# Optimization experiments

Hardware: AMD Instinct MI355X
Metric: run time of the kernel (lower is better)

Reference implementation:

```python
import jax, jax.numpy as jnp
import numpy as np
from jax import lax

# ---- config (mirrors cfg) ----
NUM_LEVELS = 4
DS = 2            # DS_FACTOR
T = 16            # TILE_SIZE
SR = 4            # SEARCH_RADIUS
PADD = 1
SW = 0.1          # SPATIAL_WEIGHT
GR = 2            # GAUSS_RADIUS
SIGMA = 1.0
SS = 2 * (SR + PADD) + 1      # 11: padded search grid
SSC = 2 * SR + 1              # 9: cropped search grid
WIN = T + 2 * (SR + PADD)     # 26: gathered window per tile

# ---- subpixel-refinement quadratic-fit filters (from __init__) ----
F_A11 = jnp.asarray(np.array([[1,-2,1],[2,-4,2],[1,-2,1]], np.float32) / 4.0)
F_A22 = jnp.asarray(np.array([[1,2,1],[-2,-4,-2],[1,2,1]], np.float32) / 4.0)
F_A12 = jnp.asarray(np.array([[1,0,-1],[0,0,0],[-1,0,1]], np.float32) / 4.0)
F_B1  = jnp.asarray(np.array([[-1,0,1],[-2,0,2],[-1,0,1]], np.float32) / 8.0)
F_B2  = jnp.asarray(np.array([[-1,-2,-1],[0,0,0],[1,2,1]], np.float32) / 8.0)
F_C   = jnp.asarray(np.array([[-1,2,-1],[2,12,2],[-1,2,-1]], np.float32) / 16.0)


def _gauss_kernel():
    ws = 2 * GR + 1
    ax = np.arange(ws, dtype=np.float32) - GR
    g = np.exp(-(ax ** 2) / (2.0 * SIGMA ** 2))
    k = np.outer(g, g)
    k = k / k.sum()
    return jnp.asarray(k, jnp.float32)


def _pyramid(x):
    """Gaussian pyramid: depthwise gaussian blur + avg-pool(ds) per level."""
    k = _gauss_kernel()[None, None]  # OIHW, C=1
    pad = (2 * GR + 1 - 1) // 2
    pyr = [x]
    for _ in range(NUM_LEVELS - 1):
        y = lax.conv_general_dilated(x, k, (1, 1), [(pad, pad), (pad, pad)],
                                     dimension_numbers=('NCHW', 'OIHW', 'NCHW'))
        n, c, h, w = y.shape
        x = y.reshape(n, c, h // DS, DS, w // DS, DS).mean(axis=(3, 5))
        pyr.append(x)
    return pyr


def _sdist_map():
    ax = (np.arange(SS, dtype=np.float32) - (SR + PADD)) / float(SS)
    return jnp.asarray(ax[:, None] ** 2 + ax[None, :] ** 2, jnp.float32)


def _step(init_offset, src, dst):
    """One pyramid-level block-matching step + subpixel refine."""
    n, nth, ntw, _ = init_offset.shape
    H, W = src.shape[2], src.shape[3]
    oy = jnp.round(init_offset[..., 0]).astype(jnp.int32)
    ox = jnp.round(init_offset[..., 1]).astype(jnp.int32)
    base_y = (jnp.arange(nth, dtype=jnp.int32) * T)[None, :, None]
    base_x = (jnp.arange(ntw, dtype=jnp.int32) * T)[None, None, :]
    y0 = base_y + oy - (SR + PADD)
    x0 = base_x + ox - (SR + PADD)
    Y = jnp.clip(y0[..., None] + jnp.arange(WIN), 0, H - 1)
    X = jnp.clip(x0[..., None] + jnp.arange(WIN), 0, W - 1)
    nidx = jnp.arange(n)[:, None, None, None, None]
    window = dst[:, 0][nidx, Y[..., :, None], X[..., None, :]]
    # source tiles [n,nth,ntw,T,T]
    src_t = src[:, 0].reshape(n, nth, T, ntw, T).transpose(0, 1, 3, 2, 4)
    # all SSxSS candidate tiles from the window (static slide indices)
    sl = jnp.arange(SS)[:, None] + jnp.arange(T)[None, :]  # [SS,T]
    cand = window[:, :, :, sl[:, None, :, None], sl[None, :, None, :]]  # [n,nth,ntw,SS,SS,T,T]
    adist = jnp.mean((cand - src_t[:, :, :, None, None]) ** 2, axis=(-2, -1))
    dist_full = adist + SW * _sdist_map()  # [n,nth,ntw,SS,SS]
    dist = dist_full[:, :, :, PADD:-PADD, PADD:-PADD].reshape(n, nth, ntw, SSC * SSC)
    min_dist = jnp.min(dist, axis=3)
    pk = jnp.argmin(dist, axis=3)
    py = pk // SSC
    px = pk % SSC
    offset = init_offset + jnp.stack([(py - SR).astype(jnp.float32),
                                      (px - SR).astype(jnp.float32)], axis=3)
    # RegionSelection: 3x3 neighborhood of dist_full around (py+PADD, px+PADD)
    ry = (py + PADD)[..., None] + jnp.arange(-1, 2)
    rx = (px + PADD)[..., None] + jnp.arange(-1, 2)
    tyi = jnp.arange(nth)[None, :, None, None, None]
    txi = jnp.arange(ntw)[None, None, :, None, None]
    yreg = dist_full[nidx, tyi, txi, ry[..., :, None], rx[..., None, :]]  # [n,nth,ntw,3,3]
    s = lambda f: jnp.sum(f * yreg, axis=(-2, -1))
    a11 = jax.nn.relu(s(F_A11))
    a22 = jax.nn.relu(s(F_A22))
    a12 = s(F_A12)
    b1 = s(F_B1)
    b2 = s(F_B2)
    det = a11 * a22 - a12 ** 2
    a12z = jnp.where(det < 0, jnp.zeros_like(a12), a12)
    mu_x = -(a22 * b1 - a12z * b2) / det
    mu_y = -(a11 * b2 - a12z * b1) / det
    mu_len = jnp.sqrt(mu_y ** 2 + mu_x ** 2)
    dx = jnp.where(mu_len < 1.0, mu_x, jnp.zeros_like(mu_x))
    dy = jnp.where(mu_len < 1.0, mu_y, jnp.zeros_like(mu_y))
    offset = offset.at[..., 0].add(dy).at[..., 1].add(dx)
    return offset, min_dist


def _inherit(prev_offset, nth, ntw, H, W):
    typ = jnp.arange(nth) // DS
    txp = jnp.arange(ntw) // DS
    off = DS * prev_offset[:, typ[:, None], txp[None, :], :]
    iy = (jnp.arange(nth, dtype=jnp.float32) * T)[None, :, None]
    ix = (jnp.arange(ntw, dtype=jnp.float32) * T)[None, None, :]
    dy = jnp.clip(off[..., 0] + iy, 0.0, float(H - T)) - iy
    dx = jnp.clip(off[..., 1] + ix, 0.0, float(W - T)) - ix
    return jnp.round(jnp.stack([dy, dx], axis=3))


def _align(src, dst):
    ps = _pyramid(src)
    pd = _pyramid(dst)
    offset = None
    min_dist = None
    for level in range(NUM_LEVELS - 1, -1, -1):
        s, d = ps[level], pd[level]
        n, _, h, w = s.shape
        nth = int(np.ceil(h / T))
        ntw = int(np.ceil(w / T))
        if level == NUM_LEVELS - 1:
            init = jnp.zeros((n, nth, ntw, 2), jnp.float32)
        else:
            init = _inherit(offset, nth, ntw, h, w)
        offset, min_dist = _step(init, s, d)
    # nearest-neighbor upsample by TILE_SIZE to per-pixel maps
    pixel_off = jnp.repeat(jnp.repeat(offset, T, axis=1), T, axis=2)   # [n,H,W,2]
    pixel_dist = jnp.repeat(jnp.repeat(min_dist, T, axis=1), T, axis=2)  # [n,H,W]
    return pixel_off, pixel_dist


def setup_inputs() -> dict:
    key = jax.random.key(0)
    k1, k2 = jax.random.split(key)
    src = jax.random.uniform(k1, (4, 1, 512, 512), jnp.float32)
    dst = jax.random.uniform(k2, (4, 1, 512, 512), jnp.float32)
    return {"src": src, "dst": dst}


def reference(src, dst):
    return _align(src, dst)
```

## Files before the change

### kernel.cpp

```cpp
#include <hip/hip_runtime.h>


#define NB 4

constexpr float H6[6] = {
    0.027244342f, 0.149345013f, 0.323410645f,
    0.323410645f, 0.149345013f, 0.027244342f
};

__global__ void __launch_bounds__(256, 2)
pyramid_kernel(const float* __restrict__ src, const float* __restrict__ dst,
               float* __restrict__ ws) {
    __shared__ float smem[14652];
    float* patch = smem;
    float* tmpH  = smem + 9900;
    float* l1    = smem;
    float* tmpB  = smem + 2256;
    float* l2    = smem + 9900;
    float* tmp3  = smem + 3384;

    float* sL1 = ws;
    float* dL1 = sL1 + 4 * 65536;
    float* sL2 = dL1 + 4 * 65536;
    float* dL2 = sL2 + 4 * 16384;
    float* sL3 = dL2 + 4 * 16384;
    float* dL3 = sL3 + 4 * 4096;

    const int bx = blockIdx.x, by = blockIdx.y, z = blockIdx.z;
    const int t = threadIdx.x;

    const float* in = (z < 4) ? (src + (size_t)z * 262144) : (dst + (size_t)(z - 4) * 262144);
    float* outL1 = ((z < 4) ? sL1 : dL1) + (size_t)(z & 3) * 65536;
    float* outL2 = ((z < 4) ? sL2 : dL2) + (size_t)(z & 3) * 16384;
    float* outL3 = ((z < 4) ? sL3 : dL3) + (size_t)(z & 3) * 4096;

    {
        const int oy = by * 64 - 14, ox = bx * 64 - 14;
        for (int idx = t; idx < 99 * 99; idx += 256) {
            int r = idx / 99, c = idx - r * 99;
            int gy = oy + r, gx = ox + c;
            float v = 0.0f;
            if (gy >= 0 && gy < 512 && gx >= 0 && gx < 512) v = in[gy * 512 + gx];
            patch[r * 100 + c] = v;
        }
    }
    __syncthreads();
    for (int idx = t; idx < 99 * 47; idx += 256) {
        int r = idx / 47, v = idx - r * 47;
        const float* p = &patch[r * 100 + 2 * v];
        float a = 0.f;
        #pragma unroll
        for (int b = 0; b < 6; ++b) a = fmaf(H6[b], p[b], a);
        tmpH[r * 48 + v] = a;
    }
    __syncthreads();
    {
        const int oy = by * 32 - 6, ox = bx * 32 - 6;
        for (int idx = t; idx < 47 * 47; idx += 256) {
            int u = idx / 47, v = idx - u * 47;
            float a = 0.f;
            int y1 = oy + u, x1 = ox + v;
            if (y1 >= 0 && y1 < 256 && x1 >= 0 && x1 < 256) {
                #pragma unroll
                for (int b = 0; b < 6; ++b) a = fmaf(H6[b], tmpH[(2 * u + b) * 48 + v], a);
            }
            l1[u * 48 + v] = a;
        }
    }
    __syncthreads();
    for (int idx = t; idx < 1024; idx += 256) {
        int u = idx >> 5, v = idx & 31;
        outL1[(by * 32 + u) * 256 + bx * 32 + v] = l1[(6 + u) * 48 + 6 + v];
    }
    for (int idx = t; idx < 47 * 21; idx += 256) {
        int r = idx / 21, v = idx - r * 21;
        const float* p = &l1[r * 48 + 2 * v];
        float a = 0.f;
        #pragma unroll
        for (int b = 0; b < 6; ++b) a = fmaf(H6[b], p[b], a);
        tmpB[r * 24 + v] = a;
    }
    __syncthreads();
    {
        const int oy = by * 16 - 2, ox = bx * 16 - 2;
        for (int idx = t; idx < 21 * 21; idx += 256) {
            int u = idx / 21, v = idx - u * 21;
            float a = 0.f;
            int y2 = oy + u, x2 = ox + v;
            if (y2 >= 0 && y2 < 128 && x2 >= 0 && x2 < 128) {
                #pragma unroll
                for (int b = 0; b < 6; ++b) a = fmaf(H6[b], tmpB[(2 * u + b) * 24 + v], a);
            }
            l2[u * 24 + v] = a;
        }
    }
    __syncthreads();
    for (int idx = t; idx < 256; idx += 256) {
        int u = idx >> 4, v = idx & 15;
        outL2[(by * 16 + u) * 128 + bx * 16 + v] = l2[(2 + u) * 24 + 2 + v];
    }
    for (int idx = t; idx < 21 * 8; idx += 256) {
        int r = idx >> 3, v = idx & 7;
        const float* p = &l2[r * 24 + 2 * v];
        float a = 0.f;
        #pragma unroll
        for (int b = 0; b < 6; ++b) a = fmaf(H6[b], p[b], a);
        tmp3[r * 8 + v] = a;
    }
    __syncthreads();
    if (t < 64) {
        int u = t >> 3, v = t & 7;
        float a = 0.f;
        #pragma unroll
        for (int b = 0; b < 6; ++b) a = fmaf(H6[b], tmp3[(2 * u + b) * 8 + v], a);
        outL3[(by * 8 + u) * 64 + bx * 8 + v] = a;
    }
}

__global__ void __launch_bounds__(256, 4)
step_chain_kernel(const float* __restrict__ src, const float* __restrict__ dst,
                  const float* __restrict__ ws, float* __restrict__ out) {
    __shared__ float winS[2][26 * 28];
    __shared__ float stS[2][256];
    __shared__ float distS[2][128];
    __shared__ float offLv[4][2];
    __shared__ float resY[2], resX[2], resD[2];

    const float* sL1 = ws;
    const float* dL1 = sL1 + 4 * 65536;
    const float* sL2 = dL1 + 4 * 65536;
    const float* dL2 = sL2 + 4 * 16384;
    const float* sL3 = dL2 + 4 * 16384;
    const float* dL3 = sL3 + 4 * 4096;

    const int gid = blockIdx.x;
    const int b   = gid >> 8;
    const int ty1 = (gid >> 4) & 15;
    const int tx1 = gid & 15;
    const int t    = threadIdx.x;
    const int slot = t >> 7;
    const int s_t  = t & 127;
    const int NPIX = NB * 512 * 512;

    float* win  = winS[slot];
    float* st   = stS[slot];
    float* dist = distS[slot];

    #pragma unroll 1
    for (int round = 0; round < 5; ++round) {
        int lvl, ty, tx; bool act, hasPar;
        const float* simg; const float* dimg; int H;
        switch (round) {
            case 0: lvl = 3; ty = ty1 >> 2; tx = tx1 >> 2; act = (slot == 0); hasPar = false; break;
            case 1: lvl = 2; ty = ty1 >> 1; tx = tx1 >> 1; act = (slot == 0); hasPar = true;  break;
            case 2: lvl = 1; ty = ty1;      tx = tx1;      act = (slot == 0); hasPar = true;  break;
            case 3: lvl = 0; ty = 2 * ty1;     tx = 2 * tx1 + slot; act = true; hasPar = true; break;
            default:lvl = 0; ty = 2 * ty1 + 1; tx = 2 * tx1 + slot; act = true; hasPar = true; break;
        }
        switch (lvl) {
            case 0: simg = src + (size_t)b * 262144; dimg = dst + (size_t)b * 262144; H = 512; break;
            case 1: simg = sL1 + (size_t)b * 65536;  dimg = dL1 + (size_t)b * 65536;  H = 256; break;
            case 2: simg = sL2 + (size_t)b * 16384;  dimg = dL2 + (size_t)b * 16384;  H = 128; break;
            default:simg = sL3 + (size_t)b * 4096;   dimg = dL3 + (size_t)b * 4096;   H = 64;  break;
        }

        float dyf = 0.f, dxf = 0.f;
        if (hasPar) {
            float poy = offLv[lvl + 1][0], pox = offLv[lvl + 1][1];
            float iy = (float)(ty * 16), ix = (float)(tx * 16);
            dyf = rintf(fminf(fmaxf(2.f * poy + iy, 0.f), (float)(H - 16)) - iy);
            dxf = rintf(fminf(fmaxf(2.f * pox + ix, 0.f), (float)(H - 16)) - ix);
        }
        const int ioy = (int)dyf, iox = (int)dxf;

        if (act) {
            const int y0 = ty * 16 + ioy - 5;
            const int x0 = tx * 16 + iox - 5;
            for (int idx = s_t; idx < 26 * 26; idx += 128) {
                int r = idx / 26, c = idx - r * 26;
                int gy = min(max(y0 + r, 0), H - 1);
                int gx = min(max(x0 + c, 0), H - 1);
                win[r * 28 + c] = dimg[gy * H + gx];
            }
            if (s_t < 64) {
                int r = s_t >> 2, q = s_t & 3;
                const float4* srow = (const float4*)(simg + (size_t)(ty * 16 + r) * H + tx * 16);
                ((float4*)&st[r * 16])[q] = srow[q];
            }
        }
        __syncthreads();

        if (act) {
            const int dy = s_t >> 3;
            const int dyc = min(dy, 10);
            float acc[11];
            #pragma unroll
            for (int q = 0; q < 11; ++q) acc[q] = 0.f;
            #pragma unroll
            for (int rr = 0; rr < 2; ++rr) {
                const int i = (s_t & 7) * 2 + rr;
                float w[28], s[16];
                const float4* wp = (const float4*)&win[(dyc + i) * 28];
                #pragma unroll
                for (int q = 0; q < 7; ++q) {
                    float4 v = wp[q];
                    w[4 * q] = v.x; w[4 * q + 1] = v.y; w[4 * q + 2] = v.z; w[4 * q + 3] = v.w;
                }
                const float4* sp = (const float4*)&st[i * 16];
                #pragma unroll
                for (int q = 0; q < 4; ++q) {
                    float4 v = sp[q];
                    s[4 * q] = v.x; s[4 * q + 1] = v.y; s[4 * q + 2] = v.z; s[4 * q + 3] = v.w;
                }
                #pragma unroll
                for (int dx = 0; dx < 11; ++dx) {
                    #pragma unroll
                    for (int j = 0; j < 16; ++j) {
                        float d = w[dx + j] - s[j];
                        acc[dx] = fmaf(d, d, acc[dx]);
                    }
                }
            }
            #pragma unroll
            for (int m = 1; m <= 4; m <<= 1) {
                #pragma unroll
                for (int dx = 0; dx < 11; ++dx) acc[dx] += __shfl_xor(acc[dx], m);
            }
            if ((s_t & 7) == 0 && dy < 11) {
                float ay = (float)(dy - 5) * (1.f / 11.f);
                #pragma unroll
                for (int dx = 0; dx < 11; ++dx) {
                    float ax = (float)(dx - 5) * (1.f / 11.f);
                    dist[dy * 11 + dx] = acc[dx] * (1.f / 256.f) + 0.1f * (ay * ay + ax * ax);
                }
            }
        }
        __syncthreads();

        if (act && s_t < 64) {
            float bv = 3e38f; int bk = 1 << 30;
            {
                int k = s_t;
                if (k < 81) {
                    int py = k / 9, px = k - (k / 9) * 9;
                    bv = dist[(py + 1) * 11 + (px + 1)]; bk = k;
                }
                k = s_t + 64;
                if (k < 81) {
                    int py = k / 9, px = k - (k / 9) * 9;
                    float d = dist[(py + 1) * 11 + (px + 1)];
                    if (d < bv || (d == bv && k < bk)) { bv = d; bk = k; }
                }
            }
            #pragma unroll
            for (int sft = 32; sft > 0; sft >>= 1) {
                float ov = __shfl_down(bv, sft);
                int   ok = __shfl_down(bk, sft);
                if (ov < bv || (ov == bv && ok < bk)) { bv = ov; bk = ok; }
            }
            if (s_t == 0) {
                int py = bk / 9, px = bk - py * 9;
                float y00 = dist[(py + 0) * 11 + (px + 0)], y01 = dist[(py + 0) * 11 + (px + 1)], y02 = dist[(py + 0) * 11 + (px + 2)];
                float y10 = dist[(py + 1) * 11 + (px + 0)],                                       y12 = dist[(py + 1) * 11 + (px + 2)];
                float y11 = dist[(py + 1) * 11 + (px + 1)];
                float y20 = dist[(py + 2) * 11 + (px + 0)], y21 = dist[(py + 2) * 11 + (px + 1)], y22 = dist[(py + 2) * 11 + (px + 2)];

                float a11 = (y00 - 2.f * y01 + y02 + 2.f * y10 - 4.f * y11 + 2.f * y12 + y20 - 2.f * y21 + y22) * 0.25f;
                a11 = fmaxf(a11, 0.f);
                float a22 = (y00 + 2.f * y01 + y02 - 2.f * y10 - 4.f * y11 - 2.f * y12 + y20 + 2.f * y21 + y22) * 0.25f;
                a22 = fmaxf(a22, 0.f);
                float a12 = (y00 - y02 - y20 + y22) * 0.25f;
                float b1  = (-y00 + y02 - 2.f * y10 + 2.f * y12 - y20 + y22) * 0.125f;
                float b2  = (-y00 - 2.f * y01 - y02 + y20 + 2.f * y21 + y22) * 0.125f;

                float det  = a11 * a22 - a12 * a12;
                float a12z = (det < 0.f) ? 0.f : a12;
                float mu_x = -(a22 * b1 - a12z * b2) / det;
                float mu_y = -(a11 * b2 - a12z * b1) / det;
                float mu_len = sqrtf(mu_x * mu_x + mu_y * mu_y);
                float addx = (mu_len < 1.f) ? mu_x : 0.f;
                float addy = (mu_len < 1.f) ? mu_y : 0.f;

                float oy = dyf + (float)(py - 4) + addy;
                float ox = dxf + (float)(px - 4) + addx;
                if (lvl > 0) { offLv[lvl][0] = oy; offLv[lvl][1] = ox; }
                resY[slot] = oy; resX[slot] = ox; resD[slot] = bv;
            }
        }
        __syncthreads();

        if (lvl == 0) {
            float2 o; o.x = resY[slot]; o.y = resX[slot];
            float2 dd; dd.x = resD[slot]; dd.y = resD[slot];
            int r = s_t >> 3, c = (s_t & 7) * 2;
            int py = ty * 16 + r, px = tx * 16 + c;
            size_t pi = ((size_t)(b * 512 + py)) * 512 + px;
            ((float2*)out)[pi]     = o;
            ((float2*)out)[pi + 1] = o;
            *(float2*)(out + (size_t)NPIX * 2 + pi) = dd;
            __syncthreads();
        }
    }
}

extern "C" void kernel_launch(void* const* d_in, const int* in_sizes, int n_in,
                              void* d_out, int out_size, void* d_ws, size_t ws_size,
                              hipStream_t stream) {
    const float* src = (const float*)d_in[0];
    const float* dst = (const float*)d_in[1];
    float* out = (float*)d_out;
    float* ws  = (float*)d_ws;

    hipLaunchKernelGGL(pyramid_kernel, dim3(8, 8, 8), dim3(256), 0, stream, src, dst, ws);
    hipLaunchKernelGGL(step_chain_kernel, dim3(1024), dim3(256), 0, stream, src, dst, ws, out);
}
```

Before: 114.7 us.

## Split pyramid into smaller tiles and use all threads for coarse matching levels

```diff
diff --git a/kernel.cpp b/kernel.cpp
--- a/kernel.cpp
+++ b/kernel.cpp
@@ -2,22 +2,23 @@
 
 
 #define NB 4
+#define NPIX (NB * 512 * 512)
 
 constexpr float H6[6] = {
     0.027244342f, 0.149345013f, 0.323410645f,
     0.323410645f, 0.149345013f, 0.027244342f
 };
 
-__global__ void __launch_bounds__(256, 2)
+__global__ void __launch_bounds__(256, 4)
 pyramid_kernel(const float* __restrict__ src, const float* __restrict__ dst,
                float* __restrict__ ws) {
-    __shared__ float smem[14652];
+    __shared__ float smem[5520];
     float* patch = smem;
-    float* tmpH  = smem + 9900;
+    float* tmpH1 = smem + 3840;
     float* l1    = smem;
-    float* tmpB  = smem + 2256;
-    float* l2    = smem + 9900;
-    float* tmp3  = smem + 3384;
+    float* tmpH2 = smem + 784;
+    float* l2    = smem + 1120;
+    float* tmpH3 = smem + 1264;
 
     float* sL1 = ws;
     float* dL1 = sL1 + 4 * 65536;
@@ -28,92 +29,212 @@
 
     const int bx = blockIdx.x, by = blockIdx.y, z = blockIdx.z;
     const int t = threadIdx.x;
-
     const float* in = (z < 4) ? (src + (size_t)z * 262144) : (dst + (size_t)(z - 4) * 262144);
-    float* outL1 = ((z < 4) ? sL1 : dL1) + (size_t)(z & 3) * 65536;
-    float* outL2 = ((z < 4) ? sL2 : dL2) + (size_t)(z & 3) * 16384;
-    float* outL3 = ((z < 4) ? sL3 : dL3) + (size_t)(z & 3) * 4096;
-
-    {
-        const int oy = by * 64 - 14, ox = bx * 64 - 14;
-        for (int idx = t; idx < 99 * 99; idx += 256) {
-            int r = idx / 99, c = idx - r * 99;
+    float* oL1 = ((z < 4) ? sL1 : dL1) + (size_t)(z & 3) * 65536;
+    float* oL2 = ((z < 4) ? sL2 : dL2) + (size_t)(z & 3) * 16384;
+    float* oL3 = ((z < 4) ? sL3 : dL3) + (size_t)(z & 3) * 4096;
+
+    {
+        const int oy = by * 32 - 14, ox = bx * 32 - 14;
+        for (int idx = t; idx < 3600; idx += 256) {
+            int r = idx / 60, c = idx - r * 60;
             int gy = oy + r, gx = ox + c;
-            float v = 0.0f;
-            if (gy >= 0 && gy < 512 && gx >= 0 && gx < 512) v = in[gy * 512 + gx];
-            patch[r * 100 + c] = v;
-        }
-    }
-    __syncthreads();
-    for (int idx = t; idx < 99 * 47; idx += 256) {
-        int r = idx / 47, v = idx - r * 47;
-        const float* p = &patch[r * 100 + 2 * v];
+            float v = 0.f;
+            if ((unsigned)gy < 512u && (unsigned)gx < 512u) v = in[gy * 512 + gx];
+            patch[r * 64 + c] = v;
+        }
+    }
+    __syncthreads();
+    for (int idx = t; idx < 1680; idx += 256) {
+        int r = idx / 28, v = idx - r * 28;
+        const float* p = &patch[r * 64 + 2 * v];
         float a = 0.f;
         #pragma unroll
-        for (int b = 0; b < 6; ++b) a = fmaf(H6[b], p[b], a);
-        tmpH[r * 48 + v] = a;
-    }
-    __syncthreads();
-    {
-        const int oy = by * 32 - 6, ox = bx * 32 - 6;
-        for (int idx = t; idx < 47 * 47; idx += 256) {
-            int u = idx / 47, v = idx - u * 47;
+        for (int bq = 0; bq < 6; ++bq) a = fmaf(H6[bq], p[bq], a);
+        tmpH1[r * 28 + v] = a;
+    }
+    __syncthreads();
+    {
+        const int oy = by * 16 - 6, ox = bx * 16 - 6;
+        for (int idx = t; idx < 784; idx += 256) {
+            int u = idx / 28, v = idx - u * 28;
             float a = 0.f;
             int y1 = oy + u, x1 = ox + v;
-            if (y1 >= 0 && y1 < 256 && x1 >= 0 && x1 < 256) {
+            if ((unsigned)y1 < 256u && (unsigned)x1 < 256u) {
                 #pragma unroll
-                for (int b = 0; b < 6; ++b) a = fmaf(H6[b], tmpH[(2 * u + b) * 48 + v], a);
+                for (int bq = 0; bq < 6; ++bq) a = fmaf(H6[bq], tmpH1[(2 * u + bq) * 28 + v], a);
             }
-            l1[u * 48 + v] = a;
-        }
-    }
-    __syncthreads();
-    for (int idx = t; idx < 1024; idx += 256) {
-        int u = idx >> 5, v = idx & 31;
-        outL1[(by * 32 + u) * 256 + bx * 32 + v] = l1[(6 + u) * 48 + 6 + v];
-    }
-    for (int idx = t; idx < 47 * 21; idx += 256) {
-        int r = idx / 21, v = idx - r * 21;
-        const float* p = &l1[r * 48 + 2 * v];
+            l1[u * 28 + v] = a;
+        }
+    }
+    __syncthreads();
+    {
+        int u = t >> 4, v = t & 15;
+        oL1[(by * 16 + u) * 256 + bx * 16 + v] = l1[(6 + u) * 28 + 6 + v];
+    }
+    for (int idx = t; idx < 336; idx += 256) {
+        int r = idx / 12, v = idx - r * 12;
+        const float* p = &l1[r * 28 + 2 * v];
         float a = 0.f;
         #pragma unroll
-        for (int b = 0; b < 6; ++b) a = fmaf(H6[b], p[b], a);
-        tmpB[r * 24 + v] = a;
-    }
-    __syncthreads();
-    {
-        const int oy = by * 16 - 2, ox = bx * 16 - 2;
-        for (int idx = t; idx < 21 * 21; idx += 256) {
-            int u = idx / 21, v = idx - u * 21;
+        for (int bq = 0; bq < 6; ++bq) a = fmaf(H6[bq], p[bq], a);
+        tmpH2[r * 12 + v] = a;
+    }
+    __syncthreads();
+    {
+        const int oy = by * 8 - 2, ox = bx * 8 - 2;
+        if (t < 144) {
+            int u = t / 12, v = t - u * 12;
             float a = 0.f;
             int y2 = oy + u, x2 = ox + v;
-            if (y2 >= 0 && y2 < 128 && x2 >= 0 && x2 < 128) {
+            if ((unsigned)y2 < 128u && (unsigned)x2 < 128u) {
                 #pragma unroll
-                for (int b = 0; b < 6; ++b) a = fmaf(H6[b], tmpB[(2 * u + b) * 24 + v], a);
+                for (int bq = 0; bq < 6; ++bq) a = fmaf(H6[bq], tmpH2[(2 * u + bq) * 12 + v], a);
             }
-            l2[u * 24 + v] = a;
-        }
-    }
-    __syncthreads();
-    for (int idx = t; idx < 256; idx += 256) {
-        int u = idx >> 4, v = idx & 15;
-        outL2[(by * 16 + u) * 128 + bx * 16 + v] = l2[(2 + u) * 24 + 2 + v];
-    }
-    for (int idx = t; idx < 21 * 8; idx += 256) {
-        int r = idx >> 3, v = idx & 7;
-        const float* p = &l2[r * 24 + 2 * v];
-        float a = 0.f;
-        #pragma unroll
-        for (int b = 0; b < 6; ++b) a = fmaf(H6[b], p[b], a);
-        tmp3[r * 8 + v] = a;
+            l2[u * 12 + v] = a;
+        }
     }
     __syncthreads();
     if (t < 64) {
         int u = t >> 3, v = t & 7;
+        oL2[(by * 8 + u) * 128 + bx * 8 + v] = l2[(2 + u) * 12 + 2 + v];
+    } else if (t < 112) {
+        int idx = t - 64;
+        int r = idx >> 2, v = idx & 3;
+        const float* p = &l2[r * 12 + 2 * v];
         float a = 0.f;
         #pragma unroll
-        for (int b = 0; b < 6; ++b) a = fmaf(H6[b], tmp3[(2 * u + b) * 8 + v], a);
-        outL3[(by * 8 + u) * 64 + bx * 8 + v] = a;
+        for (int bq = 0; bq < 6; ++bq) a = fmaf(H6[bq], p[bq], a);
+        tmpH3[r * 4 + v] = a;
+    }
+    __syncthreads();
+    if (t < 16) {
+        int u = t >> 2, v = t & 3;
+        float a = 0.f;
+        #pragma unroll
+        for (int bq = 0; bq < 6; ++bq) a = fmaf(H6[bq], tmpH3[(2 * u + bq) * 4 + v], a);
+        oL3[(by * 4 + u) * 64 + bx * 4 + v] = a;
+    }
+}
+
+template<bool FULL>
+__device__ __forceinline__ void do_level(const float* __restrict__ simg,
+                                         const float* __restrict__ dimg, int H,
+                                         int ty, int tx, float pary, float parx, bool first,
+                                         float* win, float* st, float* dist, int lt,
+                                         float& roy, float& rox, float& rod) {
+    constexpr int NL = FULL ? 256 : 128;
+
+    float dyf = 0.f, dxf = 0.f;
+    if (!first) {
+        float iy = (float)(ty * 16), ix = (float)(tx * 16);
+        dyf = rintf(fminf(fmaxf(2.f * pary + iy, 0.f), (float)(H - 16)) - iy);
+        dxf = rintf(fminf(fmaxf(2.f * parx + ix, 0.f), (float)(H - 16)) - ix);
+    }
+    const int ioy = (int)dyf, iox = (int)dxf;
+    const int y0 = ty * 16 + ioy - 5;
+    const int x0 = tx * 16 + iox - 5;
+
+    for (int idx = lt; idx < 676; idx += NL) {
+        int r = idx / 26, c = idx - r * 26;
+        int gy = min(max(y0 + r, 0), H - 1);
+        int gx = min(max(x0 + c, 0), H - 1);
+        win[r * 28 + c] = dimg[gy * H + gx];
+    }
+    if (lt < 64) {
+        int r = lt >> 2, q = lt & 3;
+        const float4* srow = (const float4*)(simg + (size_t)(ty * 16 + r) * H + tx * 16);
+        ((float4*)&st[r * 16])[q] = srow[q];
+    }
+    __syncthreads();
+
+    const int dy = FULL ? (lt >> 4) : (lt >> 3);
+    if (dy < 11) {
+        float acc[11];
+        #pragma unroll
+        for (int q = 0; q < 11; ++q) acc[q] = 0.f;
+        constexpr int ROWS = FULL ? 1 : 2;
+        #pragma unroll
+        for (int rr = 0; rr < ROWS; ++rr) {
+            const int i = FULL ? (lt & 15) : ((lt & 7) * 2 + rr);
+            float w[28], s[16];
+            const float4* wp = (const float4*)&win[(dy + i) * 28];
+            #pragma unroll
+            for (int q = 0; q < 7; ++q) ((float4*)w)[q] = wp[q];
+            const float4* sp = (const float4*)&st[i * 16];
+            #pragma unroll
+            for (int q = 0; q < 4; ++q) ((float4*)s)[q] = sp[q];
+            #pragma unroll
+            for (int dx = 0; dx < 11; ++dx) {
+                #pragma unroll
+                for (int j = 0; j < 16; ++j) {
+                    float d = w[dx + j] - s[j];
+                    acc[dx] = fmaf(d, d, acc[dx]);
+                }
+            }
+        }
+        constexpr int MMAX = FULL ? 8 : 4;
+        #pragma unroll
+        for (int m = 1; m <= MMAX; m <<= 1) {
+            #pragma unroll
+            for (int dx = 0; dx < 11; ++dx) acc[dx] += __shfl_xor(acc[dx], m);
+        }
+        const bool leader = FULL ? ((lt & 15) == 0) : ((lt & 7) == 0);
+        if (leader) {
+            float ay = (float)(dy - 5) * (1.f / 11.f);
+            #pragma unroll
+            for (int dx = 0; dx < 11; ++dx) {
+                float ax = (float)(dx - 5) * (1.f / 11.f);
+                dist[dy * 11 + dx] = acc[dx] * (1.f / 256.f) + 0.1f * (ay * ay + ax * ax);
+            }
+        }
+    }
+    __syncthreads();
+
+    const int l = lt & 63;
+    float bv; int bk;
+    {
+        int k = l;
+        int py = k / 9, px = k - (k / 9) * 9;
+        bv = dist[(py + 1) * 11 + (px + 1)]; bk = k;
+        k = l + 64;
+        if (k < 81) {
+            py = k / 9; px = k - (k / 9) * 9;
+            float d = dist[(py + 1) * 11 + (px + 1)];
+            if (d < bv) { bv = d; bk = k; }
+        }
+    }
+    #pragma unroll
+    for (int m = 1; m <= 32; m <<= 1) {
+        float ov = __shfl_xor(bv, m);
+        int   ok = __shfl_xor(bk, m);
+        if (ov < bv || (ov == bv && ok < bk)) { bv = ov; bk = ok; }
+    }
+    {
+        int py = bk / 9, px = bk - (bk / 9) * 9;
+        float y00 = dist[(py + 0) * 11 + (px + 0)], y01 = dist[(py + 0) * 11 + (px + 1)], y02 = dist[(py + 0) * 11 + (px + 2)];
+        float y10 = dist[(py + 1) * 11 + (px + 0)], y11 = dist[(py + 1) * 11 + (px + 1)], y12 = dist[(py + 1) * 11 + (px + 2)];
+        float y20 = dist[(py + 2) * 11 + (px + 0)], y21 = dist[(py + 2) * 11 + (px + 1)], y22 = dist[(py + 2) * 11 + (px + 2)];
+
+        float a11 = (y00 - 2.f * y01 + y02 + 2.f * y10 - 4.f * y11 + 2.f * y12 + y20 - 2.f * y21 + y22) * 0.25f;
+        a11 = fmaxf(a11, 0.f);
+        float a22 = (y00 + 2.f * y01 + y02 - 2.f * y10 - 4.f * y11 - 2.f * y12 + y20 + 2.f * y21 + y22) * 0.25f;
+        a22 = fmaxf(a22, 0.f);
+        float a12 = (y00 - y02 - y20 + y22) * 0.25f;
+        float b1  = (-y00 + y02 - 2.f * y10 + 2.f * y12 - y20 + y22) * 0.125f;
+        float b2  = (-y00 - 2.f * y01 - y02 + y20 + 2.f * y21 + y22) * 0.125f;
+
+        float det  = a11 * a22 - a12 * a12;
+        float a12z = (det < 0.f) ? 0.f : a12;
+        float mu_x = -(a22 * b1 - a12z * b2) / det;
+        float mu_y = -(a11 * b2 - a12z * b1) / det;
+        float mu_len = sqrtf(mu_x * mu_x + mu_y * mu_y);
+        float addx = (mu_len < 1.f) ? mu_x : 0.f;
+        float addy = (mu_len < 1.f) ? mu_y : 0.f;
+
+        roy = dyf + (float)(py - 4) + addy;
+        rox = dxf + (float)(px - 4) + addx;
+        rod = bv;
     }
 }
 
@@ -123,8 +244,6 @@
     __shared__ float winS[2][26 * 28];
     __shared__ float stS[2][256];
     __shared__ float distS[2][128];
-    __shared__ float offLv[4][2];
-    __shared__ float resY[2], resX[2], resD[2];
 
     const float* sL1 = ws;
     const float* dL1 = sL1 + 4 * 65536;
@@ -140,166 +259,34 @@
     const int t    = threadIdx.x;
     const int slot = t >> 7;
     const int s_t  = t & 127;
-    const int NPIX = NB * 512 * 512;
-
-    float* win  = winS[slot];
-    float* st   = stS[slot];
-    float* dist = distS[slot];
-
-    #pragma unroll 1
-    for (int round = 0; round < 5; ++round) {
-        int lvl, ty, tx; bool act, hasPar;
-        const float* simg; const float* dimg; int H;
-        switch (round) {
-            case 0: lvl = 3; ty = ty1 >> 2; tx = tx1 >> 2; act = (slot == 0); hasPar = false; break;
-            case 1: lvl = 2; ty = ty1 >> 1; tx = tx1 >> 1; act = (slot == 0); hasPar = true;  break;
-            case 2: lvl = 1; ty = ty1;      tx = tx1;      act = (slot == 0); hasPar = true;  break;
-            case 3: lvl = 0; ty = 2 * ty1;     tx = 2 * tx1 + slot; act = true; hasPar = true; break;
-            default:lvl = 0; ty = 2 * ty1 + 1; tx = 2 * tx1 + slot; act = true; hasPar = true; break;
-        }
-        switch (lvl) {
-            case 0: simg = src + (size_t)b * 262144; dimg = dst + (size_t)b * 262144; H = 512; break;
-            case 1: simg = sL1 + (size_t)b * 65536;  dimg = dL1 + (size_t)b * 65536;  H = 256; break;
-            case 2: simg = sL2 + (size_t)b * 16384;  dimg = dL2 + (size_t)b * 16384;  H = 128; break;
-            default:simg = sL3 + (size_t)b * 4096;   dimg = dL3 + (size_t)b * 4096;   H = 64;  break;
-        }
-
-        float dyf = 0.f, dxf = 0.f;
-        if (hasPar) {
-            float poy = offLv[lvl + 1][0], pox = offLv[lvl + 1][1];
-            float iy = (float)(ty * 16), ix = (float)(tx * 16);
-            dyf = rintf(fminf(fmaxf(2.f * poy + iy, 0.f), (float)(H - 16)) - iy);
-            dxf = rintf(fminf(fmaxf(2.f * pox + ix, 0.f), (float)(H - 16)) - ix);
-        }
-        const int ioy = (int)dyf, iox = (int)dxf;
-
-        if (act) {
-            const int y0 = ty * 16 + ioy - 5;
-            const int x0 = tx * 16 + iox - 5;
-            for (int idx = s_t; idx < 26 * 26; idx += 128) {
-                int r = idx / 26, c = idx - r * 26;
-                int gy = min(max(y0 + r, 0), H - 1);
-                int gx = min(max(x0 + c, 0), H - 1);
-                win[r * 28 + c] = dimg[gy * H + gx];
-            }
-            if (s_t < 64) {
-                int r = s_t >> 2, q = s_t & 3;
-                const float4* srow = (const float4*)(simg + (size_t)(ty * 16 + r) * H + tx * 16);
-                ((float4*)&st[r * 16])[q] = srow[q];
-            }
-        }
-        __syncthreads();
-
-        if (act) {
-            const int dy = s_t >> 3;
-            const int dyc = min(dy, 10);
-            float acc[11];
-            #pragma unroll
-            for (int q = 0; q < 11; ++q) acc[q] = 0.f;
-            #pragma unroll
-            for (int rr = 0; rr < 2; ++rr) {
-                const int i = (s_t & 7) * 2 + rr;
-                float w[28], s[16];
-                const float4* wp = (const float4*)&win[(dyc + i) * 28];
-                #pragma unroll
-                for (int q = 0; q < 7; ++q) {
-                    float4 v = wp[q];
-                    w[4 * q] = v.x; w[4 * q + 1] = v.y; w[4 * q + 2] = v.z; w[4 * q + 3] = v.w;
-                }
-                const float4* sp = (const float4*)&st[i * 16];
-                #pragma unroll
-                for (int q = 0; q < 4; ++q) {
-                    float4 v = sp[q];
-                    s[4 * q] = v.x; s[4 * q + 1] = v.y; s[4 * q + 2] = v.z; s[4 * q + 3] = v.w;
-                }
-                #pragma unroll
-                for (int dx = 0; dx < 11; ++dx) {
-                    #pragma unroll
-                    for (int j = 0; j < 16; ++j) {
-                        float d = w[dx + j] - s[j];
-                        acc[dx] = fmaf(d, d, acc[dx]);
-                    }
-                }
-            }
-            #pragma unroll
-            for (int m = 1; m <= 4; m <<= 1) {
-                #pragma unroll
-                for (int dx = 0; dx < 11; ++dx) acc[dx] += __shfl_xor(acc[dx], m);
-            }
-            if ((s_t & 7) == 0 && dy < 11) {
-                float ay = (float)(dy - 5) * (1.f / 11.f);
-                #pragma unroll
-                for (int dx = 0; dx < 11; ++dx) {
-                    float ax = (float)(dx - 5) * (1.f / 11.f);
-                    dist[dy * 11 + dx] = acc[dx] * (1.f / 256.f) + 0.1f * (ay * ay + ax * ax);
-                }
-            }
-        }
-        __syncthreads();
-
-        if (act && s_t < 64) {
-            float bv = 3e38f; int bk = 1 << 30;
-            {
-                int k = s_t;
-                if (k < 81) {
-                    int py = k / 9, px = k - (k / 9) * 9;
-                    bv = dist[(py + 1) * 11 + (px + 1)]; bk = k;
-                }
-                k = s_t + 64;
-                if (k < 81) {
-                    int py = k / 9, px = k - (k / 9) * 9;
-                    float d = dist[(py + 1) * 11 + (px + 1)];
-                    if (d < bv || (d == bv && k < bk)) { bv = d; bk = k; }
-                }
-            }
-            #pragma unroll
-            for (int sft = 32; sft > 0; sft >>= 1) {
-                float ov = __shfl_down(bv, sft);
-                int   ok = __shfl_down(bk, sft);
-                if (ov < bv || (ov == bv && ok < bk)) { bv = ov; bk = ok; }
-            }
-            if (s_t == 0) {
-                int py = bk / 9, px = bk - py * 9;
-                float y00 = dist[(py + 0) * 11 + (px + 0)], y01 = dist[(py + 0) * 11 + (px + 1)], y02 = dist[(py + 0) * 11 + (px + 2)];
-                float y10 = dist[(py + 1) * 11 + (px + 0)],                                       y12 = dist[(py + 1) * 11 + (px + 2)];
-                float y11 = dist[(py + 1) * 11 + (px + 1)];
-                float y20 = dist[(py + 2) * 11 + (px + 0)], y21 = dist[(py + 2) * 11 + (px + 1)], y22 = dist[(py + 2) * 11 + (px + 2)];
-
-                float a11 = (y00 - 2.f * y01 + y02 + 2.f * y10 - 4.f * y11 + 2.f * y12 + y20 - 2.f * y21 + y22) * 0.25f;
-                a11 = fmaxf(a11, 0.f);
-                float a22 = (y00 + 2.f * y01 + y02 - 2.f * y10 - 4.f * y11 - 2.f * y12 + y20 + 2.f * y21 + y22) * 0.25f;
-                a22 = fmaxf(a22, 0.f);
-                float a12 = (y00 - y02 - y20 + y22) * 0.25f;
-                float b1  = (-y00 + y02 - 2.f * y10 + 2.f * y12 - y20 + y22) * 0.125f;
-                float b2  = (-y00 - 2.f * y01 - y02 + y20 + 2.f * y21 + y22) * 0.125f;
-
-                float det  = a11 * a22 - a12 * a12;
-                float a12z = (det < 0.f) ? 0.f : a12;
-                float mu_x = -(a22 * b1 - a12z * b2) / det;
-                float mu_y = -(a11 * b2 - a12z * b1) / det;
-                float mu_len = sqrtf(mu_x * mu_x + mu_y * mu_y);
-                float addx = (mu_len < 1.f) ? mu_x : 0.f;
-                float addy = (mu_len < 1.f) ? mu_y : 0.f;
-
-                float oy = dyf + (float)(py - 4) + addy;
-                float ox = dxf + (float)(px - 4) + addx;
-                if (lvl > 0) { offLv[lvl][0] = oy; offLv[lvl][1] = ox; }
-                resY[slot] = oy; resX[slot] = ox; resD[slot] = bv;
-            }
-        }
-        __syncthreads();
-
-        if (lvl == 0) {
-            float2 o; o.x = resY[slot]; o.y = resX[slot];
-            float2 dd; dd.x = resD[slot]; dd.y = resD[slot];
-            int r = s_t >> 3, c = (s_t & 7) * 2;
-            int py = ty * 16 + r, px = tx * 16 + c;
-            size_t pi = ((size_t)(b * 512 + py)) * 512 + px;
-            ((float2*)out)[pi]     = o;
-            ((float2*)out)[pi + 1] = o;
-            *(float2*)(out + (size_t)NPIX * 2 + pi) = dd;
-            __syncthreads();
-        }
+
+    const float* s0 = src + (size_t)b * 262144; const float* d0 = dst + (size_t)b * 262144;
+    const float* s1 = sL1 + (size_t)b * 65536;  const float* d1 = dL1 + (size_t)b * 65536;
+    const float* s2 = sL2 + (size_t)b * 16384;  const float* d2 = dL2 + (size_t)b * 16384;
+    const float* s3 = sL3 + (size_t)b * 4096;   const float* d3 = dL3 + (size_t)b * 4096;
+
+    float oy, ox, od;
+    do_level<true>(s3, d3,  64, ty1 >> 2, tx1 >> 2, 0.f, 0.f, true,
+                   winS[0], stS[0], distS[0], t, oy, ox, od);
+    do_level<true>(s2, d2, 128, ty1 >> 1, tx1 >> 1, oy, ox, false,
+                   winS[0], stS[0], distS[0], t, oy, ox, od);
+    do_level<true>(s1, d1, 256, ty1,      tx1,      oy, ox, false,
+                   winS[0], stS[0], distS[0], t, oy, ox, od);
+    const float s1y = oy, s1x = ox;
+
+    #pragma unroll
+    for (int half = 0; half < 2; ++half) {
+        const int ty0 = 2 * ty1 + half, tx0 = 2 * tx1 + slot;
+        do_level<false>(s0, d0, 512, ty0, tx0, s1y, s1x, false,
+                        winS[slot], stS[slot], distS[slot], s_t, oy, ox, od);
+        int r = s_t >> 3, c = (s_t & 7) * 2;
+        int pyy = ty0 * 16 + r, pxx = tx0 * 16 + c;
+        size_t pi = ((size_t)(b * 512 + pyy)) * 512 + pxx;
+        float2 o; o.x = oy; o.y = ox;
+        ((float2*)out)[pi]     = o;
+        ((float2*)out)[pi + 1] = o;
+        float2 dd; dd.x = od; dd.y = od;
+        *(float2*)(out + (size_t)NPIX * 2 + pi) = dd;
     }
 }
 
@@ -311,6 +298,6 @@
     float* out = (float*)d_out;
     float* ws  = (float*)d_ws;
 
-    hipLaunchKernelGGL(pyramid_kernel, dim3(8, 8, 8), dim3(256), 0, stream, src, dst, ws);
+    hipLaunchKernelGGL(pyramid_kernel, dim3(16, 16, 8), dim3(256), 0, stream, src, dst, ws);
     hipLaunchKernelGGL(step_chain_kernel, dim3(1024), dim3(256), 0, stream, src, dst, ws, out);
 }
```

Result: faster. 112.1 us (-2.3%).
